# Optimization experiments

Measured on AMD Instinct MI355X. Metric: run time of the kernel, lower is better.

Reference implementation:

```python
import jax, jax.numpy as jnp
import numpy as np

DIM_Z, DIM_X, DIM_S = 64, 32, 16
T, N_SIMS = 1024, 1024


def _softplus_eps(x, eps=1e-6):
    return jax.nn.softplus(x) + eps


def setup_inputs() -> dict:
    key = jax.random.key(0)
    ks = jax.random.split(key, 9)
    r_z = 1.0 / np.sqrt(DIM_Z)
    r_s = 1.0 / np.sqrt(DIM_S)
    return {
        "u": jax.random.normal(ks[0], (T, N_SIMS, DIM_S), jnp.float32),
        "z0": jax.random.normal(ks[1], (N_SIMS, DIM_Z), jnp.float32),
        "noise_z": jax.random.normal(ks[2], (T, N_SIMS, DIM_Z), jnp.float32),
        "noise_x": jax.random.normal(ks[3], (T, N_SIMS, DIM_X), jnp.float32),
        "AW": jax.random.uniform(ks[4], (DIM_Z, DIM_Z), jnp.float32, -r_z, r_z),
        "C": jax.random.uniform(ks[5], (DIM_Z, DIM_S), jnp.float32, -r_s, r_s),
        "B": jax.random.uniform(ks[6], (DIM_X, DIM_Z), jnp.float32, -r_z, r_z),
        "Q": jax.random.uniform(ks[7], (DIM_Z,), jnp.float32, -0.01, 0.01),
        "R": jax.random.uniform(ks[8], (DIM_X,), jnp.float32, -0.01, 0.01),
    }


def reference(u, z0, noise_z, noise_x, AW, C, B, Q, R):
    """PF_PLRNN.simulate: T-step latent PLRNN rollout with Gaussian noise.

    z_{t+1} = A_diag*z_t + relu(z_t) @ W_off.T + u_t @ C.T + eps_z * q
    x_t     = z_t @ B.T + eps_x * r
    Returns z: (T, n_sims, d), x: (T, n_sims, p).
    """
    A_diag = jnp.diag(AW)            # (d,)
    W_off = AW - jnp.diag(A_diag)    # zero-diagonal off-part
    q = _softplus_eps(Q)             # (d,) process noise std
    r = _softplus_eps(R)             # (p,) emission noise std

    def step(z_t, inp):
        u_t, nz, nx = inp
        x_t = z_t @ B.T + nx * r                                  # (n, p)
        mu = z_t * A_diag + jax.nn.relu(z_t) @ W_off.T + u_t @ C.T  # (n, d)
        z_next = mu + nz * q
        return z_next, (z_t, x_t)

    _, (z, x) = jax.lax.scan(step, z0, (u, noise_z, noise_x))
    return z, x
```

## Files before the change

kernel.cpp:

```cpp
#include <hip/hip_runtime.h>

#define DZ 64
#define DX 32
#define DS 16
#define TT 1024
#define NS 1024

#define AW_B 0
#define C_B  (AW_B + DZ * (DZ + 1))
#define B_B  (C_B + DZ * (DS + 1))
#define SMEM_FLOATS (B_B + DX * (DZ + 1))
#define ZR_B 0
#define ZA_B 1024
#define U_B  2048

__device__ __forceinline__ float softplus_eps(float x) {
    return fmaxf(x, 0.f) + log1pf(expf(-fabsf(x))) + 1e-6f;
}

__global__ __launch_bounds__(256, 1) void plrnn_fused_kernel(
    const float* __restrict__ u,
    const float* __restrict__ z0,
    const float* __restrict__ nz,
    const float* __restrict__ nx,
    const float* __restrict__ AW,
    const float* __restrict__ Cm,
    const float* __restrict__ Bm,
    const float* __restrict__ Q,
    const float* __restrict__ R,
    float* __restrict__ zo,
    float* __restrict__ xo)
{
    const int tid  = threadIdx.x;
    const int lane = tid & 63;
    const int wv   = tid >> 6;
    const int p    = lane & 31;
    const int kb   = (lane >> 5) << 5;
    const int sim  = __builtin_amdgcn_readfirstlane((int)((blockIdx.x << 2) | wv));

    __shared__ float smem[SMEM_FLOATS];

    {
        const int r = tid >> 2;
        const int c = (tid & 3) * 16;
        #pragma unroll
        for (int k = 0; k < 16; ++k) smem[AW_B + r * (DZ + 1) + c + k] = AW[r * DZ + c + k];
        const int cc = (tid & 3) * 4;
        #pragma unroll
        for (int k = 0; k < 4; ++k) smem[C_B + r * (DS + 1) + cc + k] = Cm[r * DS + cc + k];
        const int br = tid >> 3;
        const int bc = (tid & 7) * 8;
        #pragma unroll
        for (int k = 0; k < 8; ++k) smem[B_B + br * (DZ + 1) + bc + k] = Bm[br * DZ + bc + k];
    }
    __syncthreads();

    float Wrow[DZ];
    float Ad = 0.f;
    #pragma unroll
    for (int k = 0; k < DZ; ++k) {
        const float w = smem[AW_B + lane * (DZ + 1) + k];
        Wrow[k] = (k == lane) ? 0.f : w;
        Ad      = (k == lane) ? w   : Ad;
    }
    float Crow[DS];
    #pragma unroll
    for (int s = 0; s < DS; ++s) Crow[s] = smem[C_B + lane * (DS + 1) + s];
    float Brow[32];
    #pragma unroll
    for (int k = 0; k < 32; ++k) Brow[k] = smem[B_B + p * (DZ + 1) + kb + k];

    const float qv = softplus_eps(Q[lane]);
    const float rv = softplus_eps(R[p]);

    __syncthreads();

    float zl = z0[(size_t)sim * DZ + lane];

    const size_t snz = (size_t)NS * DZ;
    const size_t snx = (size_t)NS * DX;
    const size_t su  = (size_t)NS * DS;

    const float* pnz = nz + (size_t)sim * DZ + lane;
    const float* pnx = nx + (size_t)sim * DX + p;
    const float* puu = u  + (size_t)sim * DS + (lane & 15);
    float* pz = zo + (size_t)sim * DZ + lane;
    float* px = xo + (size_t)sim * DX + p;

    float nzb[4], nxb[4], ub[4];
    #pragma unroll
    for (int j = 0; j < 4; ++j) {
        nzb[j] = pnz[(size_t)j * snz];
        nxb[j] = pnx[(size_t)j * snx];
        ub[j]  = puu[(size_t)j * su];
    }
    const float* pnz_pf = pnz + 4 * snz;
    const float* pnx_pf = pnx + 4 * snx;
    const float* puu_pf = puu + 4 * su;

    float* lzr = &smem[ZR_B + wv * DZ];
    float* lza = &smem[ZA_B + wv * DZ];
    float* lup = &smem[U_B  + wv * DS];

    for (int t0 = 0; t0 < TT; t0 += 4) {
        #pragma unroll
        for (int j = 0; j < 4; ++j) {
            const int t = t0 + j;
            const float vnz = nzb[j];
            const float vnx = nxb[j];

            lzr[lane] = zl;
            lza[lane] = fmaxf(zl, 0.f);
            if (lane < DS) lup[lane] = ub[j];

            pz[0] = zl;

            float m0 = Ad * zl, m1 = 0.f, m2 = 0.f, m3 = 0.f;

            #pragma unroll
            for (int s4 = 0; s4 < 4; ++s4) {
                const float4 uu = *(const float4*)&lup[4 * s4];
                m0 = fmaf(Crow[4*s4+0], uu.x, m0);
                m1 = fmaf(Crow[4*s4+1], uu.y, m1);
                m2 = fmaf(Crow[4*s4+2], uu.z, m2);
                m3 = fmaf(Crow[4*s4+3], uu.w, m3);
            }

            {
                const bool ok = (t + 5) < TT;
                nzb[j] = pnz_pf[0];
                nxb[j] = pnx_pf[0];
                ub[j]  = puu_pf[0];
                pnz_pf = ok ? (pnz_pf + snz) : pnz_pf;
                pnx_pf = ok ? (pnx_pf + snx) : pnx_pf;
                puu_pf = ok ? (puu_pf + su ) : puu_pf;
            }

            #pragma unroll
            for (int k4 = 0; k4 < 16; ++k4) {
                const float4 zz = *(const float4*)&lza[4 * k4];
                m0 = fmaf(Wrow[4*k4+0], zz.x, m0);
                m1 = fmaf(Wrow[4*k4+1], zz.y, m1);
                m2 = fmaf(Wrow[4*k4+2], zz.z, m2);
                m3 = fmaf(Wrow[4*k4+3], zz.w, m3);
            }

            float xa0 = 0.f, xa1 = 0.f;
            #pragma unroll
            for (int k4 = 0; k4 < 8; ++k4) {
                const float4 zz = *(const float4*)&lzr[kb + 4 * k4];
                xa0 = fmaf(Brow[4*k4+0], zz.x, xa0);
                xa1 = fmaf(Brow[4*k4+1], zz.y, xa1);
                xa0 = fmaf(Brow[4*k4+2], zz.z, xa0);
                xa1 = fmaf(Brow[4*k4+3], zz.w, xa1);
            }
            float xs = xa0 + xa1;
            xs += __shfl_xor(xs, 32);
            if (lane < DX) px[0] = fmaf(vnx, rv, xs);

            pz += snz;
            px += snx;

            zl = fmaf(vnz, qv, (m0 + m1) + (m2 + m3));
        }
    }
}

extern "C" void kernel_launch(void* const* d_in, const int* in_sizes, int n_in,
                              void* d_out, int out_size, void* d_ws, size_t ws_size,
                              hipStream_t stream) {
    const float* u_  = (const float*)d_in[0];
    const float* z0_ = (const float*)d_in[1];
    const float* nz_ = (const float*)d_in[2];
    const float* nx_ = (const float*)d_in[3];
    const float* AW_ = (const float*)d_in[4];
    const float* C_  = (const float*)d_in[5];
    const float* B_  = (const float*)d_in[6];
    const float* Q_  = (const float*)d_in[7];
    const float* R_  = (const float*)d_in[8];

    float* zo = (float*)d_out;
    float* xo = zo + (size_t)TT * NS * DZ;

    hipLaunchKernelGGL(plrnn_fused_kernel, dim3(NS / 4), dim3(256), 0, stream,
                       u_, z0_, nz_, nx_, AW_, C_, B_, Q_, R_, zo, xo);
}
```

Baseline: 513.3 us.

## Broadcast latent state via readlane instead of LDS staging

```diff
diff --git a/kernel.cpp b/kernel.cpp
--- a/kernel.cpp
+++ b/kernel.cpp
@@ -11,8 +11,6 @@
 #define B_B  (C_B + DZ * (DS + 1))
 #define SMEM_FLOATS (B_B + DX * (DZ + 1))
 #define ZR_B 0
-#define ZA_B 1024
-#define U_B  2048
 
 __device__ __forceinline__ float softplus_eps(float x) {
     return fmaxf(x, 0.f) + log1pf(expf(-fabsf(x))) + 1e-6f;
@@ -35,7 +33,6 @@
     const int lane = tid & 63;
     const int wv   = tid >> 6;
     const int p    = lane & 31;
-    const int kb   = (lane >> 5) << 5;
     const int sim  = __builtin_amdgcn_readfirstlane((int)((blockIdx.x << 2) | wv));
 
     __shared__ float smem[SMEM_FLOATS];
@@ -66,9 +63,9 @@
     float Crow[DS];
     #pragma unroll
     for (int s = 0; s < DS; ++s) Crow[s] = smem[C_B + lane * (DS + 1) + s];
-    float Brow[32];
+    float Brow[DZ];
     #pragma unroll
-    for (int k = 0; k < 32; ++k) Brow[k] = smem[B_B + p * (DZ + 1) + kb + k];
+    for (int k = 0; k < DZ; ++k) Brow[k] = smem[B_B + p * (DZ + 1) + k];
 
     const float qv = softplus_eps(Q[lane]);
     const float rv = softplus_eps(R[p]);
@@ -98,9 +95,7 @@
     const float* pnx_pf = pnx + 4 * snx;
     const float* puu_pf = puu + 4 * su;
 
-    float* lzr = &smem[ZR_B + wv * DZ];
-    float* lza = &smem[ZA_B + wv * DZ];
-    float* lup = &smem[U_B  + wv * DS];
+    volatile float* lclob = &smem[ZR_B + wv * DZ];
 
     for (int t0 = 0; t0 < TT; t0 += 4) {
         #pragma unroll
@@ -109,21 +104,26 @@
             const float vnz = nzb[j];
             const float vnx = nxb[j];
 
-            lzr[lane] = zl;
-            lza[lane] = fmaxf(zl, 0.f);
-            if (lane < DS) lup[lane] = ub[j];
+            lclob[lane] = zl;
 
             pz[0] = zl;
 
+            const int zraw = __float_as_int(zl);
+            const int uraw = __float_as_int(ub[j]);
+
             float m0 = Ad * zl, m1 = 0.f, m2 = 0.f, m3 = 0.f;
+            float xa0 = 0.f, xa1 = 0.f, xa2 = 0.f, xa3 = 0.f;
 
             #pragma unroll
-            for (int s4 = 0; s4 < 4; ++s4) {
-                const float4 uu = *(const float4*)&lup[4 * s4];
-                m0 = fmaf(Crow[4*s4+0], uu.x, m0);
-                m1 = fmaf(Crow[4*s4+1], uu.y, m1);
-                m2 = fmaf(Crow[4*s4+2], uu.z, m2);
-                m3 = fmaf(Crow[4*s4+3], uu.w, m3);
+            for (int c = 0; c < DS; c += 4) {
+                int sg0 = __builtin_amdgcn_readlane(uraw, c + 0);
+                int sg1 = __builtin_amdgcn_readlane(uraw, c + 1);
+                int sg2 = __builtin_amdgcn_readlane(uraw, c + 2);
+                int sg3 = __builtin_amdgcn_readlane(uraw, c + 3);
+                m0 = fmaf(Crow[c + 0], __int_as_float(sg0), m0);
+                m1 = fmaf(Crow[c + 1], __int_as_float(sg1), m1);
+                m2 = fmaf(Crow[c + 2], __int_as_float(sg2), m2);
+                m3 = fmaf(Crow[c + 3], __int_as_float(sg3), m3);
             }
 
             {
@@ -137,25 +137,24 @@
             }
 
             #pragma unroll
-            for (int k4 = 0; k4 < 16; ++k4) {
-                const float4 zz = *(const float4*)&lza[4 * k4];
-                m0 = fmaf(Wrow[4*k4+0], zz.x, m0);
-                m1 = fmaf(Wrow[4*k4+1], zz.y, m1);
-                m2 = fmaf(Wrow[4*k4+2], zz.z, m2);
-                m3 = fmaf(Wrow[4*k4+3], zz.w, m3);
+            for (int c = 0; c < DZ; c += 8) {
+                int sg[8];
+                #pragma unroll
+                for (int i = 0; i < 8; ++i)
+                    sg[i] = __builtin_amdgcn_readlane(zraw, c + i);
+                #pragma unroll
+                for (int i = 0; i < 8; ++i) {
+                    const int k = c + i;
+                    const float zk = __int_as_float(sg[i]);
+                    const float rk = fmaxf(zk, 0.f);
+                    if ((i & 3) == 0) { m0 = fmaf(Wrow[k], rk, m0); xa0 = fmaf(Brow[k], zk, xa0); }
+                    if ((i & 3) == 1) { m1 = fmaf(Wrow[k], rk, m1); xa1 = fmaf(Brow[k], zk, xa1); }
+                    if ((i & 3) == 2) { m2 = fmaf(Wrow[k], rk, m2); xa2 = fmaf(Brow[k], zk, xa2); }
+                    if ((i & 3) == 3) { m3 = fmaf(Wrow[k], rk, m3); xa3 = fmaf(Brow[k], zk, xa3); }
+                }
             }
 
-            float xa0 = 0.f, xa1 = 0.f;
-            #pragma unroll
-            for (int k4 = 0; k4 < 8; ++k4) {
-                const float4 zz = *(const float4*)&lzr[kb + 4 * k4];
-                xa0 = fmaf(Brow[4*k4+0], zz.x, xa0);
-                xa1 = fmaf(Brow[4*k4+1], zz.y, xa1);
-                xa0 = fmaf(Brow[4*k4+2], zz.z, xa0);
-                xa1 = fmaf(Brow[4*k4+3], zz.w, xa1);
-            }
-            float xs = xa0 + xa1;
-            xs += __shfl_xor(xs, 32);
+            const float xs = (xa0 + xa1) + (xa2 + xa3);
             if (lane < DX) px[0] = fmaf(vnx, rv, xs);
 
             pz += snz;
```

Measured after the change: 716.5 us. +39.6%, slower.

## Split each simulation's matvec reduction across two waves with per-step LDS exchange

Applied to the files above, without the earlier changes.

```diff
diff --git a/kernel.cpp b/kernel.cpp
--- a/kernel.cpp
+++ b/kernel.cpp
@@ -5,20 +5,24 @@
 #define DS 16
 #define TT 1024
 #define NS 1024
+#define SNZ (NS * DZ)
+#define SNX (NS * DX)
+#define SU4 (NS * DS / 4)
 
 #define AW_B 0
 #define C_B  (AW_B + DZ * (DZ + 1))
 #define B_B  (C_B + DZ * (DS + 1))
 #define SMEM_FLOATS (B_B + DX * (DZ + 1))
-#define ZR_B 0
-#define ZA_B 1024
-#define U_B  2048
+#define ZR_O 0
+#define RZ_O DZ
+#define PM_O (2 * DZ)
+#define PX_O (2 * DZ + 256)
 
 __device__ __forceinline__ float softplus_eps(float x) {
     return fmaxf(x, 0.f) + log1pf(expf(-fabsf(x))) + 1e-6f;
 }
 
-__global__ __launch_bounds__(256, 1) void plrnn_fused_kernel(
+__global__ __launch_bounds__(128, 2) void plrnn_split_kernel(
     const float* __restrict__ u,
     const float* __restrict__ z0,
     const float* __restrict__ nz,
@@ -33,135 +37,130 @@
 {
     const int tid  = threadIdx.x;
     const int lane = tid & 63;
-    const int wv   = tid >> 6;
+    const int kh   = tid >> 6;
     const int p    = lane & 31;
-    const int kb   = (lane >> 5) << 5;
-    const int sim  = __builtin_amdgcn_readfirstlane((int)((blockIdx.x << 2) | wv));
+    const int sim  = __builtin_amdgcn_readfirstlane((int)blockIdx.x);
 
     __shared__ float smem[SMEM_FLOATS];
 
     {
-        const int r = tid >> 2;
-        const int c = (tid & 3) * 16;
+        const int r = tid >> 1;
+        const int c = (tid & 1) * 32;
         #pragma unroll
-        for (int k = 0; k < 16; ++k) smem[AW_B + r * (DZ + 1) + c + k] = AW[r * DZ + c + k];
-        const int cc = (tid & 3) * 4;
+        for (int k = 0; k < 32; ++k) smem[AW_B + r * (DZ + 1) + c + k] = AW[r * DZ + c + k];
+        const int cc = (tid & 1) * 8;
         #pragma unroll
-        for (int k = 0; k < 4; ++k) smem[C_B + r * (DS + 1) + cc + k] = Cm[r * DS + cc + k];
-        const int br = tid >> 3;
-        const int bc = (tid & 7) * 8;
+        for (int k = 0; k < 8; ++k) smem[C_B + r * (DS + 1) + cc + k] = Cm[r * DS + cc + k];
+        const int br = tid >> 2;
+        const int bc = (tid & 3) * 16;
         #pragma unroll
-        for (int k = 0; k < 8; ++k) smem[B_B + br * (DZ + 1) + bc + k] = Bm[br * DZ + bc + k];
+        for (int k = 0; k < 16; ++k) smem[B_B + br * (DZ + 1) + bc + k] = Bm[br * DZ + bc + k];
     }
     __syncthreads();
 
-    float Wrow[DZ];
-    float Ad = 0.f;
+    float Wrow[32];
     #pragma unroll
-    for (int k = 0; k < DZ; ++k) {
+    for (int j = 0; j < 32; ++j) {
+        const int k = 32 * kh + j;
         const float w = smem[AW_B + lane * (DZ + 1) + k];
-        Wrow[k] = (k == lane) ? 0.f : w;
-        Ad      = (k == lane) ? w   : Ad;
+        Wrow[j] = (k == lane) ? 0.f : w;
     }
-    float Crow[DS];
+    const float Ad = smem[AW_B + lane * (DZ + 1) + lane];
+    float Crow[8];
     #pragma unroll
-    for (int s = 0; s < DS; ++s) Crow[s] = smem[C_B + lane * (DS + 1) + s];
-    float Brow[32];
+    for (int j = 0; j < 8; ++j) Crow[j] = smem[C_B + lane * (DS + 1) + 8 * kh + j];
+    const int kq = 32 * kh + ((lane >> 5) << 4);
+    float Brow[16];
     #pragma unroll
-    for (int k = 0; k < 32; ++k) Brow[k] = smem[B_B + p * (DZ + 1) + kb + k];
+    for (int j = 0; j < 16; ++j) Brow[j] = smem[B_B + p * (DZ + 1) + kq + j];
 
     const float qv = softplus_eps(Q[lane]);
     const float rv = softplus_eps(R[p]);
 
     __syncthreads();
 
-    float zl = z0[(size_t)sim * DZ + lane];
+    float zl = z0[sim * DZ + lane];
 
-    const size_t snz = (size_t)NS * DZ;
-    const size_t snx = (size_t)NS * DX;
-    const size_t su  = (size_t)NS * DS;
+    const float*  nzb = nz + sim * DZ;
+    const float*  nxb = nx + sim * DX;
+    const float4* ub4 = (const float4*)(u + sim * DS + 8 * kh);
+    float* zob = zo + sim * DZ;
+    float* xob = xo + sim * DX;
 
-    const float* pnz = nz + (size_t)sim * DZ + lane;
-    const float* pnx = nx + (size_t)sim * DX + p;
-    const float* puu = u  + (size_t)sim * DS + (lane & 15);
-    float* pz = zo + (size_t)sim * DZ + lane;
-    float* px = xo + (size_t)sim * DX + p;
-
-    float nzb[4], nxb[4], ub[4];
+    float nzp[4], nxp[4];
+    float4 upA[4], upB[4];
     #pragma unroll
     for (int j = 0; j < 4; ++j) {
-        nzb[j] = pnz[(size_t)j * snz];
-        nxb[j] = pnx[(size_t)j * snx];
-        ub[j]  = puu[(size_t)j * su];
+        nzp[j] = nzb[lane + j * SNZ];
+        nxp[j] = nxb[p + j * SNX];
+        upA[j] = ub4[j * SU4];
+        upB[j] = ub4[j * SU4 + 1];
     }
-    const float* pnz_pf = pnz + 4 * snz;
-    const float* pnx_pf = pnx + 4 * snx;
-    const float* puu_pf = puu + 4 * su;
-
-    float* lzr = &smem[ZR_B + wv * DZ];
-    float* lza = &smem[ZA_B + wv * DZ];
-    float* lup = &smem[U_B  + wv * DS];
 
     for (int t0 = 0; t0 < TT; t0 += 4) {
         #pragma unroll
         for (int j = 0; j < 4; ++j) {
-            const int t = t0 + j;
-            const float vnz = nzb[j];
-            const float vnx = nxb[j];
+            const int t   = t0 + j;
+            const int par = j & 1;
+            const float  vnz = nzp[j];
+            const float  vnx = nxp[j];
+            const float4 ua  = upA[j];
+            const float4 ubv = upB[j];
 
-            lzr[lane] = zl;
-            lza[lane] = fmaxf(zl, 0.f);
-            if (lane < DS) lup[lane] = ub[j];
+            smem[ZR_O + lane] = zl;
+            smem[RZ_O + lane] = fmaxf(zl, 0.f);
+            if (kh == 0) zob[lane + t * SNZ] = zl;
 
-            pz[0] = zl;
-
-            float m0 = Ad * zl, m1 = 0.f, m2 = 0.f, m3 = 0.f;
-
-            #pragma unroll
-            for (int s4 = 0; s4 < 4; ++s4) {
-                const float4 uu = *(const float4*)&lup[4 * s4];
-                m0 = fmaf(Crow[4*s4+0], uu.x, m0);
-                m1 = fmaf(Crow[4*s4+1], uu.y, m1);
-                m2 = fmaf(Crow[4*s4+2], uu.z, m2);
-                m3 = fmaf(Crow[4*s4+3], uu.w, m3);
-            }
+            float m0 = Crow[0] * ua.x,  m1 = Crow[1] * ua.y;
+            float m2 = Crow[2] * ua.z,  m3 = Crow[3] * ua.w;
+            m0 = fmaf(Crow[4], ubv.x, m0); m1 = fmaf(Crow[5], ubv.y, m1);
+            m2 = fmaf(Crow[6], ubv.z, m2); m3 = fmaf(Crow[7], ubv.w, m3);
 
             {
-                const bool ok = (t + 5) < TT;
-                nzb[j] = pnz_pf[0];
-                nxb[j] = pnx_pf[0];
-                ub[j]  = puu_pf[0];
-                pnz_pf = ok ? (pnz_pf + snz) : pnz_pf;
-                pnx_pf = ok ? (pnx_pf + snx) : pnx_pf;
-                puu_pf = ok ? (puu_pf + su ) : puu_pf;
+                int tn = t + 4; tn = (tn < TT) ? tn : (TT - 1);
+                nzp[j] = nzb[lane + tn * SNZ];
+                nxp[j] = nxb[p + tn * SNX];
+                upA[j] = ub4[tn * SU4];
+                upB[j] = ub4[tn * SU4 + 1];
             }
 
             #pragma unroll
-            for (int k4 = 0; k4 < 16; ++k4) {
-                const float4 zz = *(const float4*)&lza[4 * k4];
-                m0 = fmaf(Wrow[4*k4+0], zz.x, m0);
-                m1 = fmaf(Wrow[4*k4+1], zz.y, m1);
-                m2 = fmaf(Wrow[4*k4+2], zz.z, m2);
-                m3 = fmaf(Wrow[4*k4+3], zz.w, m3);
+            for (int k4 = 0; k4 < 8; ++k4) {
+                const float4 zz = *(const float4*)&smem[RZ_O + 32 * kh + 4 * k4];
+                m0 = fmaf(Wrow[4 * k4 + 0], zz.x, m0);
+                m1 = fmaf(Wrow[4 * k4 + 1], zz.y, m1);
+                m2 = fmaf(Wrow[4 * k4 + 2], zz.z, m2);
+                m3 = fmaf(Wrow[4 * k4 + 3], zz.w, m3);
             }
 
             float xa0 = 0.f, xa1 = 0.f;
             #pragma unroll
-            for (int k4 = 0; k4 < 8; ++k4) {
-                const float4 zz = *(const float4*)&lzr[kb + 4 * k4];
-                xa0 = fmaf(Brow[4*k4+0], zz.x, xa0);
-                xa1 = fmaf(Brow[4*k4+1], zz.y, xa1);
-                xa0 = fmaf(Brow[4*k4+2], zz.z, xa0);
-                xa1 = fmaf(Brow[4*k4+3], zz.w, xa1);
+            for (int k4 = 0; k4 < 4; ++k4) {
+                const float4 zz = *(const float4*)&smem[ZR_O + kq + 4 * k4];
+                xa0 = fmaf(Brow[4 * k4 + 0], zz.x, xa0);
+                xa1 = fmaf(Brow[4 * k4 + 1], zz.y, xa1);
+                xa0 = fmaf(Brow[4 * k4 + 2], zz.z, xa0);
+                xa1 = fmaf(Brow[4 * k4 + 3], zz.w, xa1);
             }
-            float xs = xa0 + xa1;
-            xs += __shfl_xor(xs, 32);
-            if (lane < DX) px[0] = fmaf(vnx, rv, xs);
+            float xpart = xa0 + xa1;
+            xpart += __shfl_xor(xpart, 32);
 
-            pz += snz;
-            px += snx;
+            const float mown = (m0 + m1) + (m2 + m3);
+            smem[PM_O + par * 128 + kh * 64 + lane] = mown;
+            if (kh == 0 && lane < 32) smem[PX_O + par * 32 + p] = xpart;
 
-            zl = fmaf(vnz, qv, (m0 + m1) + (m2 + m3));
+            __syncthreads();
+
+            const float moth = smem[PM_O + par * 128 + (1 - kh) * 64 + lane];
+            const float h0 = (kh == 0) ? mown : moth;
+            const float h1 = (kh == 0) ? moth : mown;
+
+            if (kh == 1 && lane < 32) {
+                const float xoth = smem[PX_O + par * 32 + p];
+                xob[p + t * SNX] = fmaf(vnx, rv, xpart + xoth);
+            }
+
+            zl = fmaf(qv, vnz, fmaf(Ad, zl, h0 + h1));
         }
     }
 }
@@ -182,6 +181,6 @@
     float* zo = (float*)d_out;
     float* xo = zo + (size_t)TT * NS * DZ;
 
-    hipLaunchKernelGGL(plrnn_fused_kernel, dim3(NS / 4), dim3(256), 0, stream,
+    hipLaunchKernelGGL(plrnn_split_kernel, dim3(NS), dim3(128), 0, stream,
                        u_, z0_, nz_, nx_, AW_, C_, B_, Q_, R_, zo, xo);
 }
```

New measurement: 456.8 us. 11.0% less time.
